# Performance work log

Hardware: AMD Instinct MI355X
Metric: run time of the kernel (lower is better)

## Reference

```python
import jax, jax.numpy as jnp
import numpy as np

B, T, C, P = 16, 8, 64, 2048
TEMP = 1.0  # init kwarg T


def setup_inputs() -> dict:
    key = jax.random.key(0)
    ks = jax.random.split(key, 16)
    shape = (B, T, C, P)
    x = jax.random.normal(ks[0], shape, dtype=jnp.float32)
    attn = jax.random.uniform(ks[1], shape, dtype=jnp.float32)
    noise = jax.random.normal(ks[2], shape, dtype=jnp.float32)
    total = B * T * C * P
    n_noisy = int(total * 0.1)  # int(0.1 * numel), as in torch code
    idx = jax.random.permutation(ks[3], total)[:n_noisy]
    mask = jnp.zeros((total,), dtype=bool).at[idx].set(True).reshape(shape)
    perms = {}
    kidx = 4
    for i in (1, 2, 3):
        for name, dim in (("pB", B), ("pT", T), ("pC", C), ("pP", P)):
            perms[f"{name}{i}"] = jax.random.permutation(ks[kidx], dim).astype(jnp.int32)
            kidx += 1
    return dict(x=x, attn=attn, noise=noise, mask=mask, **perms)


def _permute4(x, pB, pT, pC, pP):
    # equivalent to the meshgrid/flatten gather in the torch code:
    # independent permutation along each of the 4 axes
    return x[jnp.ix_(pB, pT, pC, pP)]


def reference(x, attn, noise, mask,
              pB1, pT1, pC1, pP1,
              pB2, pT2, pC2, pP2,
              pB3, pT3, pC3, pP3):
    x_pos = jnp.where(mask, x + noise, x)
    x_neg1 = _permute4(x, pB1, pT1, pC1, pP1)
    x_neg2 = _permute4(x, pB2, pT2, pC2, pP2)
    x_neg3 = _permute4(x, pB3, pT3, pC3, pP3)

    loss_pos = jnp.mean(attn * (x - x_pos) ** 2)
    loss_neg1 = jnp.mean(attn * (x - x_neg1) ** 2)
    loss_neg2 = jnp.mean(attn * (x - x_neg2) ** 2)
    loss_neg3 = jnp.mean(attn * (x - x_neg3) ** 2)

    loss = -jnp.log(jnp.exp(loss_pos / TEMP) /
                    (jnp.exp(loss_neg1 / TEMP) + jnp.exp(loss_neg2 / TEMP) + jnp.exp(loss_neg3 / TEMP)))
    return loss
```

## Files before the change

kernel.cpp:

```cpp
#include <hip/hip_runtime.h>
#include <math.h>

#define BB 16
#define TT 8
#define CC 64
#define PP 2048
#define NROWS 8192
#define RPB 4
#define NBLK (NROWS / RPB)
#define TOTAL_INV (1.0f / 16777216.0f)

typedef __attribute__((address_space(1))) const void* as1_cvoid;
typedef __attribute__((address_space(3))) void* as3_void;

__device__ __forceinline__ void stage16(const float* g, float* l) {
    __builtin_amdgcn_global_load_lds((as1_cvoid)g, (as3_void)l, 16, 0, 0);
}

__device__ __forceinline__ size_t src_of(const int* pB, const int* pT,
                                         const int* pC, int b, int t, int c) {
    return ((size_t)((pB[b] * TT + pT[t]) * CC + pC[c])) * PP;
}

__global__ __launch_bounds__(256) void mask_classify_kernel(
    const unsigned char* __restrict__ mask, int* __restrict__ flag)
{
    __shared__ int sc1, sc3f;
    if (threadIdx.x == 0) { sc1 = 0; sc3f = 0; }
    __syncthreads();
    int c1 = 0, c3f = 0;
    const uint4* m4 = (const uint4*)mask;
    for (int i = threadIdx.x; i < 1024; i += 256) {
        const uint4 v = m4[i];
        const unsigned int w[4] = {v.x, v.y, v.z, v.w};
        #pragma unroll
        for (int j = 0; j < 4; ++j) {
            #pragma unroll
            for (int bt = 0; bt < 4; ++bt) {
                const unsigned int byte = (w[j] >> (8 * bt)) & 0xffu;
                c1  += (byte == 0x01u);
                c3f += (byte == 0x3fu);
            }
        }
    }
    atomicAdd(&sc1, c1);
    atomicAdd(&sc3f, c3f);
    __syncthreads();
    if (threadIdx.x == 0) {
        int f;
        if      (sc1  > 1000) f = 0;
        else if (sc3f >  600) f = 1;
        else if (sc3f >  200) f = 2;
        else if (sc1  >  200) f = 3;
        else                  f = 0;
        *flag = f;
    }
}

template <int MODE>
__device__ __forceinline__ void mask_load(const unsigned char* __restrict__ mask,
                                          size_t idx, float mf[4])
{
    if (MODE == 0) {
        const unsigned int mv = *(const unsigned int*)(mask + idx);
        #pragma unroll
        for (int k = 0; k < 4; ++k) mf[k] = ((mv >> (8 * k)) & 0xffu) ? 1.0f : 0.0f;
    } else if (MODE == 1) {
        const ushort4 mv = *(const ushort4*)((const unsigned short*)mask + idx);
        mf[0] = mv.x ? 1.0f : 0.0f; mf[1] = mv.y ? 1.0f : 0.0f;
        mf[2] = mv.z ? 1.0f : 0.0f; mf[3] = mv.w ? 1.0f : 0.0f;
    } else if (MODE == 2) {
        const float4 mv = *(const float4*)((const float*)mask + idx);
        mf[0] = mv.x != 0.f ? 1.0f : 0.0f; mf[1] = mv.y != 0.f ? 1.0f : 0.0f;
        mf[2] = mv.z != 0.f ? 1.0f : 0.0f; mf[3] = mv.w != 0.f ? 1.0f : 0.0f;
    } else {
        const int4 mv = *(const int4*)((const int*)mask + idx);
        mf[0] = mv.x ? 1.0f : 0.0f; mf[1] = mv.y ? 1.0f : 0.0f;
        mf[2] = mv.z ? 1.0f : 0.0f; mf[3] = mv.w ? 1.0f : 0.0f;
    }
}

template <int MODE>
__device__ __forceinline__ void block_body(
    const float* __restrict__ x, const float* __restrict__ attn,
    const float* __restrict__ noise, const unsigned char* __restrict__ mask,
    const int* __restrict__ pB1, const int* __restrict__ pT1,
    const int* __restrict__ pC1, const int* __restrict__ pP1,
    const int* __restrict__ pB2, const int* __restrict__ pT2,
    const int* __restrict__ pC2, const int* __restrict__ pP2,
    const int* __restrict__ pB3, const int* __restrict__ pT3,
    const int* __restrict__ pC3, const int* __restrict__ pP3,
    float (*sbuf)[PP],
    int r0, int tid, int wave, int lane,
    float& s0, float& s1, float& s2, float& s3)
{
    #pragma unroll
    for (int i = 0; i < RPB; ++i) {
        const int r = r0 + i;
        const int b = r / (TT * CC);
        const int t = (r / CC) % TT;
        const int c = r % CC;
        const size_t a0 = src_of(pB1, pT1, pC1, b, t, c);
        const size_t a1 = src_of(pB2, pT2, pC2, b, t, c);
        const size_t a2 = src_of(pB3, pT3, pC3, b, t, c);

        #pragma unroll
        for (int s = 0; s < 2; ++s) {
            const int seg = wave + s * 4;
            const int fo  = seg * 256 + lane * 4;
            stage16(x + a0 + fo, &sbuf[0][seg * 256]);
            stage16(x + a1 + fo, &sbuf[1][seg * 256]);
            stage16(x + a2 + fo, &sbuf[2][seg * 256]);
        }

        const size_t rowbase = (size_t)r * PP;
        const int p0 = tid << 2;
        const int p1 = 1024 + (tid << 2);
        const float4 xv0 = *(const float4*)(x + rowbase + p0);
        const float4 xv1 = *(const float4*)(x + rowbase + p1);
        const float4 av0 = *(const float4*)(attn + rowbase + p0);
        const float4 av1 = *(const float4*)(attn + rowbase + p1);
        const float4 nv0 = *(const float4*)(noise + rowbase + p0);
        const float4 nv1 = *(const float4*)(noise + rowbase + p1);
        const int4 q10 = *(const int4*)(pP1 + p0);
        const int4 q11 = *(const int4*)(pP1 + p1);
        const int4 q20 = *(const int4*)(pP2 + p0);
        const int4 q21 = *(const int4*)(pP2 + p1);
        const int4 q30 = *(const int4*)(pP3 + p0);
        const int4 q31 = *(const int4*)(pP3 + p1);
        float mf0[4], mf1[4];
        mask_load<MODE>(mask, rowbase + p0, mf0);
        mask_load<MODE>(mask, rowbase + p1, mf1);

        const float as0[4]  = {av0.x, av0.y, av0.z, av0.w};
        const float as1v[4] = {av1.x, av1.y, av1.z, av1.w};

        {
            const float ns0[4] = {nv0.x, nv0.y, nv0.z, nv0.w};
            const float ns1[4] = {nv1.x, nv1.y, nv1.z, nv1.w};
            #pragma unroll
            for (int k = 0; k < 4; ++k) {
                const float d0a = ns0[k] * mf0[k];
                s0 += as0[k] * d0a * d0a;
                const float d0b = ns1[k] * mf1[k];
                s0 += as1v[k] * d0b * d0b;
            }
        }

        __syncthreads();

        const int q1s[8] = {q10.x, q10.y, q10.z, q10.w, q11.x, q11.y, q11.z, q11.w};
        const int q2s[8] = {q20.x, q20.y, q20.z, q20.w, q21.x, q21.y, q21.z, q21.w};
        const int q3s[8] = {q30.x, q30.y, q30.z, q30.w, q31.x, q31.y, q31.z, q31.w};
        float g1[8], g2[8], g3[8];
        #pragma unroll
        for (int k = 0; k < 8; ++k) g1[k] = sbuf[0][q1s[k]];
        #pragma unroll
        for (int k = 0; k < 8; ++k) g2[k] = sbuf[1][q2s[k]];
        #pragma unroll
        for (int k = 0; k < 8; ++k) g3[k] = sbuf[2][q3s[k]];
        __builtin_amdgcn_sched_barrier(0);

        {
            const float xs[8] = {xv0.x, xv0.y, xv0.z, xv0.w,
                                 xv1.x, xv1.y, xv1.z, xv1.w};
            const float aa[8] = {as0[0], as0[1], as0[2], as0[3],
                                 as1v[0], as1v[1], as1v[2], as1v[3]};
            #pragma unroll
            for (int k = 0; k < 8; ++k) {
                const float d1 = xs[k] - g1[k];
                s1 += aa[k] * d1 * d1;
                const float d2 = xs[k] - g2[k];
                s2 += aa[k] * d2 * d2;
                const float d3 = xs[k] - g3[k];
                s3 += aa[k] * d3 * d3;
            }
        }

        __syncthreads();
    }
}

__global__ __launch_bounds__(256) void attn_loss_row_kernel(
    const float* __restrict__ x, const float* __restrict__ attn,
    const float* __restrict__ noise, const unsigned char* __restrict__ mask,
    const int* __restrict__ pB1, const int* __restrict__ pT1,
    const int* __restrict__ pC1, const int* __restrict__ pP1,
    const int* __restrict__ pB2, const int* __restrict__ pT2,
    const int* __restrict__ pC2, const int* __restrict__ pP2,
    const int* __restrict__ pB3, const int* __restrict__ pT3,
    const int* __restrict__ pC3, const int* __restrict__ pP3,
    const int* __restrict__ mask_flag,
    float4* __restrict__ partial)
{
    __shared__ float sbuf[3][PP];
    __shared__ float red[4][4];

    const int tid  = threadIdx.x;
    const int wave = tid >> 6;
    const int lane = tid & 63;
    const int r0   = blockIdx.x * RPB;

    float s0 = 0.f, s1 = 0.f, s2 = 0.f, s3 = 0.f;

    const int f = *mask_flag;
    switch (f) {
        case 1:  block_body<1>(x, attn, noise, mask, pB1, pT1, pC1, pP1,
                               pB2, pT2, pC2, pP2, pB3, pT3, pC3, pP3,
                               sbuf, r0, tid, wave, lane, s0, s1, s2, s3); break;
        case 2:  block_body<2>(x, attn, noise, mask, pB1, pT1, pC1, pP1,
                               pB2, pT2, pC2, pP2, pB3, pT3, pC3, pP3,
                               sbuf, r0, tid, wave, lane, s0, s1, s2, s3); break;
        case 3:  block_body<3>(x, attn, noise, mask, pB1, pT1, pC1, pP1,
                               pB2, pT2, pC2, pP2, pB3, pT3, pC3, pP3,
                               sbuf, r0, tid, wave, lane, s0, s1, s2, s3); break;
        default: block_body<0>(x, attn, noise, mask, pB1, pT1, pC1, pP1,
                               pB2, pT2, pC2, pP2, pB3, pT3, pC3, pP3,
                               sbuf, r0, tid, wave, lane, s0, s1, s2, s3); break;
    }

    #pragma unroll
    for (int off = 32; off; off >>= 1) {
        s0 += __shfl_down(s0, off, 64);
        s1 += __shfl_down(s1, off, 64);
        s2 += __shfl_down(s2, off, 64);
        s3 += __shfl_down(s3, off, 64);
    }
    if (lane == 0) {
        red[0][wave] = s0; red[1][wave] = s1;
        red[2][wave] = s2; red[3][wave] = s3;
    }
    __syncthreads();
    if (tid == 0) {
        float4 out;
        out.x = red[0][0] + red[0][1] + red[0][2] + red[0][3];
        out.y = red[1][0] + red[1][1] + red[1][2] + red[1][3];
        out.z = red[2][0] + red[2][1] + red[2][2] + red[2][3];
        out.w = red[3][0] + red[3][1] + red[3][2] + red[3][3];
        partial[blockIdx.x] = out;
    }
}

__global__ __launch_bounds__(1024) void attn_loss_final_kernel(
    const float4* __restrict__ partial, float* __restrict__ out)
{
    const int tid = threadIdx.x;
    float s0 = 0.f, s1 = 0.f, s2 = 0.f, s3 = 0.f;
    for (int i = tid; i < NBLK; i += 1024) {
        const float4 v = partial[i];
        s0 += v.x; s1 += v.y; s2 += v.z; s3 += v.w;
    }
    #pragma unroll
    for (int off = 32; off; off >>= 1) {
        s0 += __shfl_down(s0, off, 64);
        s1 += __shfl_down(s1, off, 64);
        s2 += __shfl_down(s2, off, 64);
        s3 += __shfl_down(s3, off, 64);
    }
    __shared__ float red[4][16];
    const int wave = tid >> 6;
    const int lane = tid & 63;
    if (lane == 0) {
        red[0][wave] = s0; red[1][wave] = s1;
        red[2][wave] = s2; red[3][wave] = s3;
    }
    __syncthreads();
    if (tid == 0) {
        float lp = 0.f, l1 = 0.f, l2 = 0.f, l3 = 0.f;
        #pragma unroll
        for (int w = 0; w < 16; ++w) {
            lp += red[0][w]; l1 += red[1][w];
            l2 += red[2][w]; l3 += red[3][w];
        }
        lp *= TOTAL_INV; l1 *= TOTAL_INV; l2 *= TOTAL_INV; l3 *= TOTAL_INV;
        const float m   = fmaxf(l1, fmaxf(l2, l3));
        const float lse = m + logf(expf(l1 - m) + expf(l2 - m) + expf(l3 - m));
        out[0] = lse - lp;
    }
}

extern "C" void kernel_launch(void* const* d_in, const int* in_sizes, int n_in,
                              void* d_out, int out_size, void* d_ws, size_t ws_size,
                              hipStream_t stream) {
    const float* x            = (const float*)d_in[0];
    const float* attn         = (const float*)d_in[1];
    const float* noise        = (const float*)d_in[2];
    const unsigned char* mask = (const unsigned char*)d_in[3];
    const int* pB1 = (const int*)d_in[4];
    const int* pT1 = (const int*)d_in[5];
    const int* pC1 = (const int*)d_in[6];
    const int* pP1 = (const int*)d_in[7];
    const int* pB2 = (const int*)d_in[8];
    const int* pT2 = (const int*)d_in[9];
    const int* pC2 = (const int*)d_in[10];
    const int* pP2 = (const int*)d_in[11];
    const int* pB3 = (const int*)d_in[12];
    const int* pT3 = (const int*)d_in[13];
    const int* pC3 = (const int*)d_in[14];
    const int* pP3 = (const int*)d_in[15];

    float4* partial = (float4*)d_ws;
    int* mask_flag  = (int*)((char*)d_ws + NBLK * 16);

    mask_classify_kernel<<<1, 256, 0, stream>>>(mask, mask_flag);
    attn_loss_row_kernel<<<NBLK, 256, 0, stream>>>(
        x, attn, noise, mask,
        pB1, pT1, pC1, pP1, pB2, pT2, pC2, pP2, pB3, pT3, pC3, pP3,
        mask_flag, partial);
    attn_loss_final_kernel<<<1, 1024, 0, stream>>>(partial, (float*)d_out);
}
```

Before: 85.69 us.

## Gather permuted rows directly from global memory instead of LDS staging

Drops the global_load_lds staging of the three permuted source rows into shared memory, along with the two block barriers per row. Each thread now gathers its permuted elements straight from global memory, relying on L2/cache to absorb the scattered accesses within a 8KB row. The pP permutation loads are hoisted out of the row loop and the source offsets are precomputed, and launch bounds request higher occupancy. The cost is uncoalesced scattered global loads in place of coalesced 16-byte staging.

```diff
diff --git a/kernel.cpp b/kernel.cpp
--- a/kernel.cpp
+++ b/kernel.cpp
@@ -9,13 +9,6 @@
 #define RPB 4
 #define NBLK (NROWS / RPB)
 #define TOTAL_INV (1.0f / 16777216.0f)
-
-typedef __attribute__((address_space(1))) const void* as1_cvoid;
-typedef __attribute__((address_space(3))) void* as3_void;
-
-__device__ __forceinline__ void stage16(const float* g, float* l) {
-    __builtin_amdgcn_global_load_lds((as1_cvoid)g, (as3_void)l, 16, 0, 0);
-}
 
 __device__ __forceinline__ size_t src_of(const int* pB, const int* pT,
                                          const int* pC, int b, int t, int c) {
@@ -90,98 +83,83 @@
     const int* __restrict__ pC2, const int* __restrict__ pP2,
     const int* __restrict__ pB3, const int* __restrict__ pT3,
     const int* __restrict__ pC3, const int* __restrict__ pP3,
-    float (*sbuf)[PP],
-    int r0, int tid, int wave, int lane,
+    int r0, int tid,
     float& s0, float& s1, float& s2, float& s3)
 {
+    const int p0 = tid << 2;
+    const int p1 = 1024 + (tid << 2);
+
+    const int4 q10 = *(const int4*)(pP1 + p0);
+    const int4 q11 = *(const int4*)(pP1 + p1);
+    const int4 q20 = *(const int4*)(pP2 + p0);
+    const int4 q21 = *(const int4*)(pP2 + p1);
+    const int4 q30 = *(const int4*)(pP3 + p0);
+    const int4 q31 = *(const int4*)(pP3 + p1);
+    const int q1s[8] = {q10.x, q10.y, q10.z, q10.w, q11.x, q11.y, q11.z, q11.w};
+    const int q2s[8] = {q20.x, q20.y, q20.z, q20.w, q21.x, q21.y, q21.z, q21.w};
+    const int q3s[8] = {q30.x, q30.y, q30.z, q30.w, q31.x, q31.y, q31.z, q31.w};
+
+    size_t sA[RPB], sB[RPB], sC[RPB];
     #pragma unroll
     for (int i = 0; i < RPB; ++i) {
         const int r = r0 + i;
         const int b = r / (TT * CC);
         const int t = (r / CC) % TT;
         const int c = r % CC;
-        const size_t a0 = src_of(pB1, pT1, pC1, b, t, c);
-        const size_t a1 = src_of(pB2, pT2, pC2, b, t, c);
-        const size_t a2 = src_of(pB3, pT3, pC3, b, t, c);
-
-        #pragma unroll
-        for (int s = 0; s < 2; ++s) {
-            const int seg = wave + s * 4;
-            const int fo  = seg * 256 + lane * 4;
-            stage16(x + a0 + fo, &sbuf[0][seg * 256]);
-            stage16(x + a1 + fo, &sbuf[1][seg * 256]);
-            stage16(x + a2 + fo, &sbuf[2][seg * 256]);
-        }
-
-        const size_t rowbase = (size_t)r * PP;
-        const int p0 = tid << 2;
-        const int p1 = 1024 + (tid << 2);
+        sA[i] = src_of(pB1, pT1, pC1, b, t, c);
+        sB[i] = src_of(pB2, pT2, pC2, b, t, c);
+        sC[i] = src_of(pB3, pT3, pC3, b, t, c);
+    }
+
+    #pragma unroll
+    for (int i = 0; i < RPB; ++i) {
+        const size_t rowbase = (size_t)(r0 + i) * PP;
+        const float* __restrict__ r1 = x + sA[i];
+        const float* __restrict__ r2 = x + sB[i];
+        const float* __restrict__ r3 = x + sC[i];
+
+        float g1[8], g2[8], g3[8];
+        #pragma unroll
+        for (int k = 0; k < 8; ++k) g1[k] = r1[q1s[k]];
+        #pragma unroll
+        for (int k = 0; k < 8; ++k) g2[k] = r2[q2s[k]];
+        #pragma unroll
+        for (int k = 0; k < 8; ++k) g3[k] = r3[q3s[k]];
+
         const float4 xv0 = *(const float4*)(x + rowbase + p0);
         const float4 xv1 = *(const float4*)(x + rowbase + p1);
         const float4 av0 = *(const float4*)(attn + rowbase + p0);
         const float4 av1 = *(const float4*)(attn + rowbase + p1);
         const float4 nv0 = *(const float4*)(noise + rowbase + p0);
         const float4 nv1 = *(const float4*)(noise + rowbase + p1);
-        const int4 q10 = *(const int4*)(pP1 + p0);
-        const int4 q11 = *(const int4*)(pP1 + p1);
-        const int4 q20 = *(const int4*)(pP2 + p0);
-        const int4 q21 = *(const int4*)(pP2 + p1);
-        const int4 q30 = *(const int4*)(pP3 + p0);
-        const int4 q31 = *(const int4*)(pP3 + p1);
         float mf0[4], mf1[4];
         mask_load<MODE>(mask, rowbase + p0, mf0);
         mask_load<MODE>(mask, rowbase + p1, mf1);
-
-        const float as0[4]  = {av0.x, av0.y, av0.z, av0.w};
-        const float as1v[4] = {av1.x, av1.y, av1.z, av1.w};
-
-        {
-            const float ns0[4] = {nv0.x, nv0.y, nv0.z, nv0.w};
-            const float ns1[4] = {nv1.x, nv1.y, nv1.z, nv1.w};
-            #pragma unroll
-            for (int k = 0; k < 4; ++k) {
-                const float d0a = ns0[k] * mf0[k];
-                s0 += as0[k] * d0a * d0a;
-                const float d0b = ns1[k] * mf1[k];
-                s0 += as1v[k] * d0b * d0b;
-            }
+        __builtin_amdgcn_sched_barrier(0);
+
+        const float xs[8] = {xv0.x, xv0.y, xv0.z, xv0.w,
+                             xv1.x, xv1.y, xv1.z, xv1.w};
+        const float aa[8] = {av0.x, av0.y, av0.z, av0.w,
+                             av1.x, av1.y, av1.z, av1.w};
+        const float nn[8] = {nv0.x, nv0.y, nv0.z, nv0.w,
+                             nv1.x, nv1.y, nv1.z, nv1.w};
+        const float mm[8] = {mf0[0], mf0[1], mf0[2], mf0[3],
+                             mf1[0], mf1[1], mf1[2], mf1[3]};
+        #pragma unroll
+        for (int k = 0; k < 8; ++k) {
+            const float d0 = nn[k] * mm[k];
+            s0 += aa[k] * d0 * d0;
+            const float d1 = xs[k] - g1[k];
+            s1 += aa[k] * d1 * d1;
+            const float d2 = xs[k] - g2[k];
+            s2 += aa[k] * d2 * d2;
+            const float d3 = xs[k] - g3[k];
+            s3 += aa[k] * d3 * d3;
         }
-
-        __syncthreads();
-
-        const int q1s[8] = {q10.x, q10.y, q10.z, q10.w, q11.x, q11.y, q11.z, q11.w};
-        const int q2s[8] = {q20.x, q20.y, q20.z, q20.w, q21.x, q21.y, q21.z, q21.w};
-        const int q3s[8] = {q30.x, q30.y, q30.z, q30.w, q31.x, q31.y, q31.z, q31.w};
-        float g1[8], g2[8], g3[8];
-        #pragma unroll
-        for (int k = 0; k < 8; ++k) g1[k] = sbuf[0][q1s[k]];
-        #pragma unroll
-        for (int k = 0; k < 8; ++k) g2[k] = sbuf[1][q2s[k]];
-        #pragma unroll
-        for (int k = 0; k < 8; ++k) g3[k] = sbuf[2][q3s[k]];
-        __builtin_amdgcn_sched_barrier(0);
-
-        {
-            const float xs[8] = {xv0.x, xv0.y, xv0.z, xv0.w,
-                                 xv1.x, xv1.y, xv1.z, xv1.w};
-            const float aa[8] = {as0[0], as0[1], as0[2], as0[3],
-                                 as1v[0], as1v[1], as1v[2], as1v[3]};
-            #pragma unroll
-            for (int k = 0; k < 8; ++k) {
-                const float d1 = xs[k] - g1[k];
-                s1 += aa[k] * d1 * d1;
-                const float d2 = xs[k] - g2[k];
-                s2 += aa[k] * d2 * d2;
-                const float d3 = xs[k] - g3[k];
-                s3 += aa[k] * d3 * d3;
-            }
-        }
-
-        __syncthreads();
-    }
-}
-
-__global__ __launch_bounds__(256) void attn_loss_row_kernel(
+    }
+}
+
+__global__ __launch_bounds__(256, 4) void attn_loss_row_kernel(
     const float* __restrict__ x, const float* __restrict__ attn,
     const float* __restrict__ noise, const unsigned char* __restrict__ mask,
     const int* __restrict__ pB1, const int* __restrict__ pT1,
@@ -193,7 +171,6 @@
     const int* __restrict__ mask_flag,
     float4* __restrict__ partial)
 {
-    __shared__ float sbuf[3][PP];
     __shared__ float red[4][4];
 
     const int tid  = threadIdx.x;
@@ -207,16 +184,16 @@
     switch (f) {
         case 1:  block_body<1>(x, attn, noise, mask, pB1, pT1, pC1, pP1,
                                pB2, pT2, pC2, pP2, pB3, pT3, pC3, pP3,
-                               sbuf, r0, tid, wave, lane, s0, s1, s2, s3); break;
+                               r0, tid, s0, s1, s2, s3); break;
         case 2:  block_body<2>(x, attn, noise, mask, pB1, pT1, pC1, pP1,
                                pB2, pT2, pC2, pP2, pB3, pT3, pC3, pP3,
-                               sbuf, r0, tid, wave, lane, s0, s1, s2, s3); break;
+                               r0, tid, s0, s1, s2, s3); break;
         case 3:  block_body<3>(x, attn, noise, mask, pB1, pT1, pC1, pP1,
                                pB2, pT2, pC2, pP2, pB3, pT3, pC3, pP3,
-                               sbuf, r0, tid, wave, lane, s0, s1, s2, s3); break;
+                               r0, tid, s0, s1, s2, s3); break;
         default: block_body<0>(x, attn, noise, mask, pB1, pT1, pC1, pP1,
                                pB2, pT2, pC2, pP2, pB3, pT3, pC3, pP3,
-                               sbuf, r0, tid, wave, lane, s0, s1, s2, s3); break;
+                               r0, tid, s0, s1, s2, s3); break;
     }
 
     #pragma unroll
```

After: 184.3 us. +115.1%, slower.
